# Performance work log

Measured on AMD Instinct MI355X. Metric: run time of the kernel, lower is better.

## Reference

```python
import jax, jax.numpy as jnp
import numpy as np

B, T, D, H = 2, 2048, 1024, 32
NEG = -1e9  # used in place of -inf for masked logits (no fully-masked rows here)


def setup_inputs() -> dict:
    key = jax.random.key(0)
    ks = jax.random.split(key, 8)
    q = jax.random.normal(ks[0], (B, T, D), jnp.float32)
    k = jax.random.normal(ks[1], (B, T, D), jnp.float32)
    v = jax.random.normal(ks[2], (B, T, D), jnp.float32)
    Wqkv = jax.random.normal(ks[3], (D, 3 * D), jnp.float32) * 0.02
    bqkv = jax.random.normal(ks[4], (3 * D,), jnp.float32) * 0.02
    Wo = jax.random.normal(ks[5], (D, D), jnp.float32) * 0.02
    bo = jax.random.normal(ks[6], (D,), jnp.float32) * 0.02
    # pad the last 128 key positions of batch element 1
    key_padding_mask = jnp.zeros((B, T), bool).at[1, T - 128:].set(True)
    # causal mask: prevent attending to subsequent tokens (True = masked)
    attn_mask = jnp.triu(jnp.ones((T, T), bool), k=1)
    return {"q": q, "k": k, "v": v, "Wqkv": Wqkv, "bqkv": bqkv,
            "Wo": Wo, "bo": bo, "key_padding_mask": key_padding_mask,
            "attn_mask": attn_mask, "n_heads": H}


def reference(q, k, v, Wqkv, bqkv, Wo, bo, key_padding_mask, attn_mask, n_heads):
    Bq, T1, Dm = q.shape
    T2 = k.shape[1]
    dh = Dm // n_heads
    # project concatenated [q; k; v] tokens with the shared qkv Linear
    x = jnp.concatenate([q, k, v], axis=1)                 # [B, T1+2*T2, D]
    proj = x @ Wqkv + bqkv                                 # [B, Ttot, 3D]
    # channel layout is (qkv h d) per the Rearrange
    proj = proj.reshape(Bq, -1, 3, n_heads, dh)            # [B, Ttot, 3, H, dh]
    qp = proj[:, :T1, 0]                                   # [B, T1, H, dh]
    kp = proj[:, T1:T1 + T2, 1]                            # [B, T2, H, dh]
    vp = proj[:, T1 + T2:, 2]                              # [B, T2, H, dh]
    scores = jnp.einsum('bqhd,bkhd->bhqk', qp, kp) / np.sqrt(dh).astype(qp.dtype)
    mask = key_padding_mask[:, None, None, :] | attn_mask[None, None, :, :]
    scores = jnp.where(mask, NEG, scores)
    attn = jax.nn.softmax(scores, axis=-1)                 # [B, H, T1, T2]
    y = jnp.einsum('bhqk,bkhd->bqhd', attn, vp)            # [B, T1, H, dh]
    y = y.reshape(Bq, T1, Dm)
    return y @ Wo + bo
```

## Files before the change

### kernel.cpp

```cpp
#include <hip/hip_runtime.h>

typedef __bf16 bf16;
typedef __bf16 bf16x4 __attribute__((ext_vector_type(4)));
typedef __bf16 bf16x8 __attribute__((ext_vector_type(8)));
typedef float  f32x4  __attribute__((ext_vector_type(4)));

#define MFMA16(A, B, C) __builtin_amdgcn_mfma_f32_16x16x32_bf16((A), (B), (C), 0, 0, 0)

__device__ __forceinline__ void gld16(void* lds, const void* g) {
  __builtin_amdgcn_global_load_lds((__attribute__((address_space(1))) void*)(g),
                                   (__attribute__((address_space(3))) void*)(lds),
                                   16, 0, 0);
}

__global__ __launch_bounds__(256) void prep(const float* __restrict__ q,
                                            const float* __restrict__ k,
                                            const float* __restrict__ v,
                                            bf16* __restrict__ d,
                                            const float* __restrict__ Wqkv,
                                            bf16* __restrict__ Wt,
                                            const float* __restrict__ Wo,
                                            bf16* __restrict__ Wot) {
  __shared__ float t[32][33];
  int bi = blockIdx.x;
  if (bi < 6144) {
    int which = bi >> 11;
    const float* s = (which == 0) ? q : ((which == 1) ? k : v);
    int i = ((bi & 2047) * 256 + threadIdx.x) * 8;
    float4 a = *(const float4*)&s[i];
    float4 b = *(const float4*)&s[i + 4];
    bf16x8 o;
    o[0] = (bf16)a.x; o[1] = (bf16)a.y; o[2] = (bf16)a.z; o[3] = (bf16)a.w;
    o[4] = (bf16)b.x; o[5] = (bf16)b.y; o[6] = (bf16)b.z; o[7] = (bf16)b.w;
    *(bf16x8*)&d[(size_t)which * 4194304 + i] = o;
    return;
  }
  const float* W; bf16* WT; int Nc, bx_, by_;
  if (bi < 9216) {
    int idx = bi - 6144;
    W = Wqkv; WT = Wt; Nc = 3072; bx_ = idx % 96; by_ = idx / 96;
  } else {
    int idx = bi - 9216;
    W = Wo; WT = Wot; Nc = 1024; bx_ = idx & 31; by_ = idx >> 5;
  }
  const int Kr = 1024;
  int n0 = bx_ * 32, k0 = by_ * 32;
  int tx = threadIdx.x & 31, ty = threadIdx.x >> 5;
  #pragma unroll
  for (int i = 0; i < 4; ++i)
    t[ty + i * 8][tx] = W[(size_t)(k0 + ty + i * 8) * Nc + n0 + tx];
  __syncthreads();
  #pragma unroll
  for (int i = 0; i < 4; ++i)
    WT[(size_t)(n0 + ty + i * 8) * Kr + k0 + tx] = (bf16)t[tx][ty + i * 8];
}

template <int MODE, int BN>
__global__ __launch_bounds__(256) void gemm_bt(const bf16* __restrict__ Ab,
                                               const bf16* __restrict__ Btb,
                                               const float* __restrict__ biasb,
                                               void* __restrict__ outp, int K) {
  constexpr int NI = BN / 32;
  __shared__ bf16 lA[128 * 32];
  __shared__ bf16 lB[BN * 32];
  const int z = blockIdx.z;
  const bf16* A  = Ab  + (size_t)z * 4096 * 1024;
  const bf16* Bt = Btb + (size_t)z * 1024 * 1024;
  const float* bias = biasb + z * 1024;
  const int m0 = blockIdx.y * 128, n0 = blockIdx.x * BN;
  const int tid = threadIdx.x;
  const int w = tid >> 6, lane = tid & 63, g = lane >> 4, c = lane & 15;
  const int wm = (w & 1) * 64, wn = (w >> 1) * (BN / 2);
  const int srow = tid >> 2;
  const int skq  = (tid & 3) * 8;

  f32x4 acc[4][NI] = {};

  for (int k0 = 0; k0 < K; k0 += 32) {
    gld16(&lA[srow * 32 + skq],        &A [(size_t)(m0 + srow)      * K + k0 + skq]);
    gld16(&lA[(64 + srow) * 32 + skq], &A [(size_t)(m0 + 64 + srow) * K + k0 + skq]);
    gld16(&lB[srow * 32 + skq],        &Bt[(size_t)(n0 + srow)      * K + k0 + skq]);
    if constexpr (BN > 64)
      gld16(&lB[(64 + srow) * 32 + skq], &Bt[(size_t)(n0 + 64 + srow) * K + k0 + skq]);
    __syncthreads();
    bf16x8 af[4], bf_[NI];
    #pragma unroll
    for (int i = 0; i < 4; ++i)
      af[i]  = *(const bf16x8*)&lA[(wm + i * 16 + c) * 32 + g * 8];
    #pragma unroll
    for (int i = 0; i < NI; ++i)
      bf_[i] = *(const bf16x8*)&lB[(wn + i * 16 + c) * 32 + g * 8];
    #pragma unroll
    for (int mi = 0; mi < 4; ++mi)
      #pragma unroll
      for (int ni = 0; ni < NI; ++ni)
        acc[mi][ni] = MFMA16(af[mi], bf_[ni], acc[mi][ni]);
    __syncthreads();
  }

  float bv[NI];
  #pragma unroll
  for (int ni = 0; ni < NI; ++ni) bv[ni] = bias[n0 + wn + ni * 16 + c];

  if constexpr (MODE == 0) {
    bf16* O = (bf16*)outp;
    if (z == 2) {
      #pragma unroll
      for (int mi = 0; mi < 4; ++mi) {
        int mg0 = m0 + wm + mi * 16 + g * 4;
        int bb = mg0 >> 11, tt = mg0 & 2047;
        #pragma unroll
        for (int ni = 0; ni < NI; ++ni) {
          int col = n0 + wn + ni * 16 + c;
          bf16x4 pv;
          #pragma unroll
          for (int r = 0; r < 4; ++r) pv[r] = (bf16)(acc[mi][ni][r] + bv[ni]);
          size_t off = ((((size_t)(4 + bb) * 32 + (col >> 5)) * 32) + (col & 31)) * 2048 + tt;
          *(bf16x4*)&O[off] = pv;
        }
      }
    } else {
      const float scale = (z == 0) ? 0.2550353720f : 1.0f;
      #pragma unroll
      for (int mi = 0; mi < 4; ++mi) {
        #pragma unroll
        for (int r = 0; r < 4; ++r) {
          int mg = m0 + wm + mi * 16 + g * 4 + r;
          int bb = mg >> 11, tt = mg & 2047;
          #pragma unroll
          for (int ni = 0; ni < NI; ++ni) {
            int col = n0 + wn + ni * 16 + c;
            float val = (acc[mi][ni][r] + bv[ni]) * scale;
            size_t off = ((((size_t)z * 2 + bb) * 32 + (col >> 5)) * 2048 + tt) * 32 + (col & 31);
            O[off] = (bf16)val;
          }
        }
      }
    }
  } else {
    float* O = (float*)outp;
    #pragma unroll
    for (int mi = 0; mi < 4; ++mi) {
      #pragma unroll
      for (int r = 0; r < 4; ++r) {
        int mg = m0 + wm + mi * 16 + g * 4 + r;
        #pragma unroll
        for (int ni = 0; ni < NI; ++ni) {
          int col = n0 + wn + ni * 16 + c;
          O[(size_t)mg * 1024 + col] = acc[mi][ni][r] + bv[ni];
        }
      }
    }
  }
}

__global__ __launch_bounds__(256, 4) void attn(const bf16* __restrict__ qkvp,
                                               bf16* __restrict__ Y) {
  __shared__ bf16 KL[4][64 * 32];
  __shared__ bf16 P[4][16 * 72];

  const int bh = blockIdx.x, b = bh >> 5, h = bh & 31;
  const int bx = blockIdx.y;
  const int qtA = bx, qtB = 31 - bx;
  const int tid = threadIdx.x, w = tid >> 6, lane = tid & 63, g = lane >> 4, c = lane & 15;

  const bf16* Qh = qkvp + ((size_t)b * 32 + h) * 65536;
  const bf16* Kh = qkvp + ((size_t)(2 + b) * 32 + h) * 65536;
  const bf16* Vh = qkvp + ((size_t)(4 + b) * 32 + h) * 65536;

  const int qrowA = qtA * 64 + w * 16 + c;
  const int qrowB = qtB * 64 + w * 16 + c;
  const bf16x8 qfA = *(const bf16x8*)&Qh[(size_t)qrowA * 32 + g * 8];
  const bf16x8 qfB = *(const bf16x8*)&Qh[(size_t)qrowB * 32 + g * 8];

  bf16x8 ones;
  #pragma unroll
  for (int j = 0; j < 8; ++j) ones[j] = (bf16)1.0f;

  f32x4 oA0 = {}, oA1 = {}, osA = {};
  f32x4 oB0 = {}, oB1 = {}, osB = {};
  float mA = -1e30f, mB = -1e30f;

  const int ksr = tid >> 2, ksc = (tid & 3) * 8;
  bf16* Pw = &P[w][0];

  auto k_stage = [&](int kt) {
    gld16(&KL[kt & 3][ksr * 32 + ksc], &Kh[(size_t)(kt * 64 + ksr) * 32 + ksc]);
  };
  auto kfrag = [&](int kt, bf16x8* kf) {
    #pragma unroll
    for (int t = 0; t < 4; ++t)
      kf[t] = *(const bf16x8*)&KL[kt & 3][(t * 16 + c) * 32 + g * 8];
  };
  auto ld_v = [&](int kt, bf16x8* vf) {
    const bf16* Vt = Vh + kt * 64;
    vf[0] = *(const bf16x8*)&Vt[(size_t)c * 2048 + g * 8];
    vf[1] = *(const bf16x8*)&Vt[(size_t)c * 2048 + 32 + g * 8];
    vf[2] = *(const bf16x8*)&Vt[(size_t)(16 + c) * 2048 + g * 8];
    vf[3] = *(const bf16x8*)&Vt[(size_t)(16 + c) * 2048 + 32 + g * 8];
  };
  auto mask_tile = [&](f32x4* st4, int kt, int qrow, bool diag, bool pad) {
    #pragma unroll
    for (int t = 0; t < 4; ++t) {
      int kb = kt * 64 + t * 16 + g * 4;
      #pragma unroll
      for (int r = 0; r < 4; ++r) {
        int kk = kb + r;
        bool m = (diag && kk > qrow) || (pad && kk >= 1920);
        st4[t][r] = m ? -1e9f : st4[t][r];
      }
    }
  };
  auto tmax4in = [&](const f32x4* st4) -> float {
    float t0 = fmaxf(fmaxf(st4[0][0], st4[0][1]), fmaxf(st4[0][2], st4[0][3]));
    float t1 = fmaxf(fmaxf(st4[1][0], st4[1][1]), fmaxf(st4[1][2], st4[1][3]));
    float t2 = fmaxf(fmaxf(st4[2][0], st4[2][1]), fmaxf(st4[2][2], st4[2][3]));
    float t3 = fmaxf(fmaxf(st4[3][0], st4[3][1]), fmaxf(st4[3][2], st4[3][3]));
    return fmaxf(fmaxf(t0, t1), fmaxf(t2, t3));
  };
  auto xred = [&](float tm) -> float {
    tm = fmaxf(tm, __shfl_xor(tm, 16));
    return fmaxf(tm, __shfl_xor(tm, 32));
  };
  auto qk = [&](const bf16x8* kf, const bf16x8& qf, f32x4* st) {
    __builtin_amdgcn_s_setprio(1);
    #pragma unroll
    for (int t = 0; t < 4; ++t) {
      f32x4 z = {};
      st[t] = MFMA16(kf[t], qf, z);
    }
    __builtin_amdgcn_s_setprio(0);
  };
  auto p_tile = [&](const f32x4* st4, float mn) {
    #pragma unroll
    for (int t = 0; t < 4; ++t) {
      bf16x4 pv;
      #pragma unroll
      for (int r = 0; r < 4; ++r) pv[r] = (bf16)__builtin_amdgcn_exp2f(st4[t][r] - mn);
      *(bf16x4*)&Pw[c * 72 + t * 16 + g * 4] = pv;
    }
  };
  auto p_read = [&](bf16x8& pf0, bf16x8& pf1) {
    pf0 = *(const bf16x8*)&Pw[c * 72 + g * 8];
    pf1 = *(const bf16x8*)&Pw[c * 72 + 32 + g * 8];
  };
  auto rescale = [&](float a, f32x4& o0, f32x4& o1, f32x4& os) {
    #pragma unroll
    for (int r = 0; r < 4; ++r) {
      float ar = __shfl(a, g * 4 + r);
      o0[r] *= ar; o1[r] *= ar; os[r] *= ar;
    }
  };
  auto pv_mfma = [&](bf16x8 pf0, bf16x8 pf1, const bf16x8* vf,
                     f32x4& o0, f32x4& o1, f32x4& os) {
    __builtin_amdgcn_s_setprio(1);
    o0 = MFMA16(pf0, vf[0], o0);
    o0 = MFMA16(pf1, vf[1], o0);
    o1 = MFMA16(pf0, vf[2], o1);
    o1 = MFMA16(pf1, vf[3], o1);
    os = MFMA16(pf0, ones, os);
    os = MFMA16(pf1, ones, os);
    __builtin_amdgcn_s_setprio(0);
  };

  k_stage(0);
  __syncthreads();

  for (int kt = 0; kt <= qtA; ++kt) {
    k_stage(kt + 1);
    bf16x8 kf[4], vf[4];
    kfrag(kt, kf);
    ld_v(kt, vf);

    f32x4 stA[4], stB[4];
    qk(kf, qfA, stA);
    if (kt == qtA) mask_tile(stA, kt, qrowA, true, false);
    float tmA = xred(tmax4in(stA));
    bool upA = !__all(tmA <= mA + 8.f);
    float mnA = upA ? fmaxf(mA, tmA) : mA;
    p_tile(stA, mnA);
    bf16x8 pfA0, pfA1;
    p_read(pfA0, pfA1);

    qk(kf, qfB, stB);
    float tmB = xred(tmax4in(stB));
    bool upB = !__all(tmB <= mB + 8.f);
    float mnB = upB ? fmaxf(mB, tmB) : mB;
    p_tile(stB, mnB);
    bf16x8 pfB0, pfB1;
    p_read(pfB0, pfB1);

    if (upA) {
      float a = __builtin_amdgcn_exp2f(mA - mnA);
      mA = mnA;
      rescale(a, oA0, oA1, osA);
    }
    pv_mfma(pfA0, pfA1, vf, oA0, oA1, osA);
    if (upB) {
      float a = __builtin_amdgcn_exp2f(mB - mnB);
      mB = mnB;
      rescale(a, oB0, oB1, osB);
    }
    pv_mfma(pfB0, pfB1, vf, oB0, oB1, osB);
    __syncthreads();
  }

  const int s = qtA + 1;
  bf16x8 vfp[4];
  bf16x8 pfB0, pfB1;
  {
    if (s + 1 <= qtB) k_stage(s + 1);
    bf16x8 kf[4];
    kfrag(s, kf);
    ld_v(s, vfp);
    f32x4 st[4];
    qk(kf, qfB, st);
    if (s == qtB) mask_tile(st, s, qrowB, true, false);
    float tm = xred(tmax4in(st));
    bool up = !__all(tm <= mB + 8.f);
    float mn = up ? fmaxf(mB, tm) : mB;
    if (up) {
      float a = __builtin_amdgcn_exp2f(mB - mn);
      mB = mn;
      rescale(a, oB0, oB1, osB);
    }
    p_tile(st, mn);
    p_read(pfB0, pfB1);
    __syncthreads();
  }

  for (int kt = s + 1; kt <= qtB; ++kt) {
    if (kt + 1 <= qtB) k_stage(kt + 1);
    bf16x8 kf[4], vfc[4];
    kfrag(kt, kf);
    ld_v(kt, vfc);

    f32x4 st[4];
    qk(kf, qfB, st);
    const bool diag = (kt == qtB);
    const bool pad = (b == 1) && (kt >= 30);
    if (diag || pad) mask_tile(st, kt, qrowB, diag, pad);
    float tm = xred(tmax4in(st));
    bool up = !__all(tm <= mB + 8.f);
    float mn = up ? fmaxf(mB, tm) : mB;

    pv_mfma(pfB0, pfB1, vfp, oB0, oB1, osB);
    if (up) {
      float a = __builtin_amdgcn_exp2f(mB - mn);
      mB = mn;
      rescale(a, oB0, oB1, osB);
    }
    p_tile(st, mn);
    p_read(pfB0, pfB1);
    #pragma unroll
    for (int i = 0; i < 4; ++i) vfp[i] = vfc[i];
    __syncthreads();
  }

  pv_mfma(pfB0, pfB1, vfp, oB0, oB1, osB);

  #pragma unroll
  for (int r = 0; r < 4; ++r) {
    float li = 1.f / osB[r];
    int qg = qtB * 64 + w * 16 + g * 4 + r;
    size_t base = ((size_t)b * 2048 + qg) * 1024 + h * 32;
    Y[base + c]      = (bf16)(oB0[r] * li);
    Y[base + 16 + c] = (bf16)(oB1[r] * li);
  }
  #pragma unroll
  for (int r = 0; r < 4; ++r) {
    float li = 1.f / osA[r];
    int qg = qtA * 64 + w * 16 + g * 4 + r;
    size_t base = ((size_t)b * 2048 + qg) * 1024 + h * 32;
    Y[base + c]      = (bf16)(oA0[r] * li);
    Y[base + 16 + c] = (bf16)(oA1[r] * li);
  }
}

extern "C" void kernel_launch(void* const* d_in, const int* in_sizes, int n_in,
                              void* d_out, int out_size, void* d_ws, size_t ws_size,
                              hipStream_t stream) {
  const float* q    = (const float*)d_in[0];
  const float* k    = (const float*)d_in[1];
  const float* v    = (const float*)d_in[2];
  const float* Wqkv = (const float*)d_in[3];
  const float* bqkv = (const float*)d_in[4];
  const float* Wo   = (const float*)d_in[5];
  const float* bo   = (const float*)d_in[6];

  bf16* xqkv = (bf16*)d_ws;
  bf16* Wt   = xqkv + 12582912;
  bf16* Wot  = Wt + 3145728;
  bf16* qkvp = Wot + 1048576;
  bf16* Yb   = qkvp + 12582912;

  prep<<<10240, 256, 0, stream>>>(q, k, v, xqkv, Wqkv, Wt, Wo, Wot);
  gemm_bt<0, 128><<<dim3(8, 32, 3), 256, 0, stream>>>(xqkv, Wt, bqkv, (void*)qkvp, 1024);
  attn<<<dim3(64, 16), 256, 0, stream>>>(qkvp, Yb);
  gemm_bt<1, 64><<<dim3(16, 32, 1), 256, 0, stream>>>(Yb, Wot, bo, d_out, 1024);
}
```

Before: 247.4 us.

## Stage V tiles through swizzled LDS and process two key tiles per iteration

V fragments now go through LDS using async global-to-LDS loads with an XOR swizzle, instead of being read directly from global memory with strided accesses. K staging gets a matching swizzle to cut bank conflicts. The tail loop over the B query tile now handles two key tiles per iteration with one shared max reduction and rescale, which drops the software-pipelined P/V carry. The cost is extra LDS use and extra barriers around the V staging, which may reduce occupancy and add stalls.

```diff
diff --git a/kernel.cpp b/kernel.cpp
--- a/kernel.cpp
+++ b/kernel.cpp
@@ -157,6 +157,7 @@
 __global__ __launch_bounds__(256, 4) void attn(const bf16* __restrict__ qkvp,
                                                bf16* __restrict__ Y) {
   __shared__ bf16 KL[4][64 * 32];
+  __shared__ bf16 VL[2][32 * 64];
   __shared__ bf16 P[4][16 * 72];
 
   const int bh = blockIdx.x, b = bh >> 5, h = bh & 31;
@@ -181,23 +182,33 @@
   f32x4 oB0 = {}, oB1 = {}, osB = {};
   float mA = -1e30f, mB = -1e30f;
 
-  const int ksr = tid >> 2, ksc = (tid & 3) * 8;
   bf16* Pw = &P[w][0];
 
+  const int ksrc = (tid * 16) ^ (((tid >> 2) & 3) << 4);
   auto k_stage = [&](int kt) {
-    gld16(&KL[kt & 3][ksr * 32 + ksc], &Kh[(size_t)(kt * 64 + ksr) * 32 + ksc]);
-  };
+    gld16(&KL[kt & 3][tid * 8], (const char*)Kh + kt * 4096 + ksrc);
+  };
+  const size_t vsrc = (size_t)(tid >> 3) * 4096 +
+                      (((tid & 7) * 16) ^ (((tid >> 3) & 7) << 4));
+  auto v_stage = [&](int kt) {
+    gld16(&VL[kt & 1][tid * 8], (const char*)Vh + vsrc + kt * 128);
+  };
+  const int kxor = (c & 3) << 4;
   auto kfrag = [&](int kt, bf16x8* kf) {
+    const char* bas = (const char*)&KL[kt & 3][0] + c * 64 + ((g * 16) ^ kxor);
     #pragma unroll
     for (int t = 0; t < 4; ++t)
-      kf[t] = *(const bf16x8*)&KL[kt & 3][(t * 16 + c) * 32 + g * 8];
-  };
-  auto ld_v = [&](int kt, bf16x8* vf) {
-    const bf16* Vt = Vh + kt * 64;
-    vf[0] = *(const bf16x8*)&Vt[(size_t)c * 2048 + g * 8];
-    vf[1] = *(const bf16x8*)&Vt[(size_t)c * 2048 + 32 + g * 8];
-    vf[2] = *(const bf16x8*)&Vt[(size_t)(16 + c) * 2048 + g * 8];
-    vf[3] = *(const bf16x8*)&Vt[(size_t)(16 + c) * 2048 + 32 + g * 8];
+      kf[t] = *(const bf16x8*)(bas + t * 1024);
+  };
+  const int vxor = (c & 7) << 4;
+  auto vfrag = [&](int kt, bf16x8* vf) {
+    const char* bas = (const char*)&VL[kt & 1][0];
+    const int o0 = c * 128 + ((g * 16) ^ vxor);
+    const int o1 = c * 128 + ((64 + g * 16) ^ vxor);
+    vf[0] = *(const bf16x8*)(bas + o0);
+    vf[1] = *(const bf16x8*)(bas + o1);
+    vf[2] = *(const bf16x8*)(bas + 2048 + o0);
+    vf[3] = *(const bf16x8*)(bas + 2048 + o1);
   };
   auto mask_tile = [&](f32x4* st4, int kt, int qrow, bool diag, bool pad) {
     #pragma unroll
@@ -264,13 +275,15 @@
   };
 
   k_stage(0);
+  v_stage(0);
   __syncthreads();
 
   for (int kt = 0; kt <= qtA; ++kt) {
     k_stage(kt + 1);
+    v_stage(kt + 1);
     bf16x8 kf[4], vf[4];
     kfrag(kt, kf);
-    ld_v(kt, vf);
+    vfrag(kt, vf);
 
     f32x4 stA[4], stB[4];
     qk(kf, qfA, stA);
@@ -306,58 +319,79 @@
   }
 
   const int s = qtA + 1;
-  bf16x8 vfp[4];
-  bf16x8 pfB0, pfB1;
   {
-    if (s + 1 <= qtB) k_stage(s + 1);
-    bf16x8 kf[4];
+    const bool more = (s < qtB);
+    if (more) { k_stage(s + 1); k_stage(s + 2); v_stage(s + 1); }
+    bf16x8 kf[4], vf[4];
     kfrag(s, kf);
-    ld_v(s, vfp);
+    vfrag(s, vf);
     f32x4 st[4];
     qk(kf, qfB, st);
     if (s == qtB) mask_tile(st, s, qrowB, true, false);
     float tm = xred(tmax4in(st));
     bool up = !__all(tm <= mB + 8.f);
     float mn = up ? fmaxf(mB, tm) : mB;
+    p_tile(st, mn);
+    bf16x8 pf0, pf1;
+    p_read(pf0, pf1);
     if (up) {
       float a = __builtin_amdgcn_exp2f(mB - mn);
       mB = mn;
       rescale(a, oB0, oB1, osB);
     }
-    p_tile(st, mn);
-    p_read(pfB0, pfB1);
-    __syncthreads();
-  }
-
-  for (int kt = s + 1; kt <= qtB; ++kt) {
-    if (kt + 1 <= qtB) k_stage(kt + 1);
-    bf16x8 kf[4], vfc[4];
-    kfrag(kt, kf);
-    ld_v(kt, vfc);
-
-    f32x4 st[4];
+    pv_mfma(pf0, pf1, vf, oB0, oB1, osB);
+    if (more) {
+      __syncthreads();
+      v_stage(s + 2);
+      __syncthreads();
+    }
+  }
+
+  for (int p = s + 1; p < qtB; p += 2) {
+    const bool f = (p + 3 <= qtB);
+    if (f) { k_stage(p + 2); k_stage(p + 3); }
+    bf16x8 kf[4], kf2[4];
+    kfrag(p, kf);
+    kfrag(p + 1, kf2);
+
+    f32x4 st[8];
     qk(kf, qfB, st);
-    const bool diag = (kt == qtB);
-    const bool pad = (b == 1) && (kt >= 30);
-    if (diag || pad) mask_tile(st, kt, qrowB, diag, pad);
-    float tm = xred(tmax4in(st));
+    qk(kf2, qfB, st + 4);
+    const bool diag2 = (p + 1 == qtB);
+    const bool pad1 = (b == 1) && (p >= 30);
+    const bool pad2 = (b == 1) && (p + 1 >= 30);
+    if (pad1) mask_tile(st, p, qrowB, false, true);
+    if (diag2 || pad2) mask_tile(st + 4, p + 1, qrowB, diag2, pad2);
+
+    float tm = xred(fmaxf(tmax4in(st), tmax4in(st + 4)));
     bool up = !__all(tm <= mB + 8.f);
     float mn = up ? fmaxf(mB, tm) : mB;
-
-    pv_mfma(pfB0, pfB1, vfp, oB0, oB1, osB);
     if (up) {
       float a = __builtin_amdgcn_exp2f(mB - mn);
       mB = mn;
       rescale(a, oB0, oB1, osB);
     }
+
+    bf16x8 vfa[4];
+    vfrag(p, vfa);
     p_tile(st, mn);
-    p_read(pfB0, pfB1);
-    #pragma unroll
-    for (int i = 0; i < 4; ++i) vfp[i] = vfc[i];
-    __syncthreads();
-  }
-
-  pv_mfma(pfB0, pfB1, vfp, oB0, oB1, osB);
+    bf16x8 pf0, pf1;
+    p_read(pf0, pf1);
+    pv_mfma(pf0, pf1, vfa, oB0, oB1, osB);
+
+    bf16x8 vfb[4];
+    vfrag(p + 1, vfb);
+    p_tile(st + 4, mn);
+    p_read(pf0, pf1);
+    pv_mfma(pf0, pf1, vfb, oB0, oB1, osB);
+
+    if (f) {
+      __syncthreads();
+      v_stage(p + 2);
+      v_stage(p + 3);
+      __syncthreads();
+    }
+  }
 
   #pragma unroll
   for (int r = 0; r < 4; ++r) {
```

Measured after the change: 233.8 us. 1.06x faster.
